# Performance work log

Measured on AMD Instinct MI355X. Metric: run time of the kernel, lower is better.

## Reference

```python
import jax, jax.numpy as jnp
import numpy as np

BATCH = 64
FEAT = 2048          # backbone.out_features (ResNet-50)
C = 112              # bottleneck_dim = number of concepts
E = 512              # concept_emb_dim
NUM_CLASSES = 345


def setup_inputs() -> dict:
    key = jax.random.key(0)
    ks = jax.random.split(key, 7)
    s_emb = 1.0 / np.sqrt(FEAT)
    s_p = 1.0 / np.sqrt(2 * E)
    s_h = 1.0 / np.sqrt(C * E)
    return {
        "x": jax.random.normal(ks[0], (BATCH, FEAT), jnp.float32),
        "W_emb": jax.random.normal(ks[1], (C, FEAT, 2 * E), jnp.float32) * s_emb,
        "b_emb": jax.random.normal(ks[2], (C, 2 * E), jnp.float32) * s_emb,
        "W_pint": jax.random.normal(ks[3], (C, 2 * E), jnp.float32) * s_p,
        "b_pint": jax.random.normal(ks[4], (C,), jnp.float32) * s_p,
        "W_head": jax.random.normal(ks[5], (C * E, NUM_CLASSES), jnp.float32) * s_h,
        "b_head": jax.random.normal(ks[6], (NUM_CLASSES,), jnp.float32) * s_h,
    }


def reference(x, W_emb, b_emb, W_pint, b_pint, W_head, b_head):
    # Batched version of the per-concept Linear loop: [B,C,2E]
    embeddings = jnp.einsum("bf,cfe->bce", x, W_emb) + b_emb
    positive_embs = embeddings[..., :E]   # [B,C,E]
    negative_embs = embeddings[..., E:]   # [B,C,E]
    # Per-concept Linear(2E, 1) -> [B,C]
    p_int_logits = jnp.einsum("bce,ce->bc", embeddings, W_pint) + b_pint
    p_int_pos = jax.nn.sigmoid(p_int_logits)              # [B,C]
    p = p_int_pos[..., None]
    mixed_embs = p * positive_embs + (1.0 - p) * negative_embs  # [B,C,E]
    flattened = mixed_embs.reshape(mixed_embs.shape[0], -1)     # [B, C*E]
    final_preds = flattened @ W_head + b_head                   # [B, num_classes]
    return (final_preds, flattened, p_int_pos)
```

## Files before the change

kernel.cpp:

```cpp
#include <hip/hip_runtime.h>

typedef __attribute__((ext_vector_type(4))) float  f4;
typedef __attribute__((ext_vector_type(8))) short  bf16x8;
typedef __attribute__((ext_vector_type(4))) float  f32x4;
typedef __attribute__((ext_vector_type(4))) unsigned short us4;
typedef __attribute__((ext_vector_type(2))) unsigned int u32x2;
typedef __attribute__((ext_vector_type(4))) unsigned int u32x4;

#define BATCH 64
#define FEAT 2048
#define NC_C 112
#define TE 1024
#define EE 512
#define NCLS 345
#define NCLSP 352
#define KHEAD 57344

__device__ __forceinline__ unsigned short f2bf(float f) {
    unsigned u = __float_as_uint(f);
    unsigned r = (u + 0x7FFFu + ((u >> 16) & 1u)) >> 16;
    return (unsigned short)r;
}
__device__ __forceinline__ float bf2f(unsigned short h) {
    return __uint_as_float(((unsigned)h) << 16);
}
__device__ __forceinline__ unsigned cvtpk(float a, float b) {
    unsigned r;
    asm("v_cvt_pk_bf16_f32 %0, %1, %2" : "=v"(r) : "v"(a), "v"(b));
    return r;
}

__global__ __launch_bounds__(256) void k_emb(
    const float* __restrict__ x, const float* __restrict__ W_emb,
    unsigned short* __restrict__ pbe)
{
    __shared__ __align__(16) unsigned short Alds[64 * 40];
    __shared__ __align__(16) unsigned short Blds[128 * 40];

    const int tid = threadIdx.x;
    const int bid = blockIdx.x;
    const int c  = bid >> 6;
    const int nt = (bid >> 3) & 7;
    const int ks = bid & 7;
    const int n0 = nt * 128;
    const int kofs = ks * 256;
    const float* __restrict__ Wc = W_emb + (size_t)c * (FEAT * TE);

    const int w = tid >> 6, l = tid & 63;
    const int mbase = (w & 1) * 32, nbase = (w >> 1) * 64;

    const int a_row = tid >> 3;
    const int a_k4  = (tid & 7) * 4;
    const int b_kp  = tid >> 4;
    const int b_n4  = (tid & 15) * 4;

    const float* __restrict__ axp = x + (size_t)a_row * FEAT + kofs + a_k4;
    const float* __restrict__ bpp = Wc + (size_t)(kofs + 2 * b_kp) * TE + n0 + b_n4;

    unsigned short* __restrict__ aw0 = &Alds[a_row * 40 + a_k4];
    unsigned short* __restrict__ aw1 = &Alds[(a_row + 32) * 40 + a_k4];
    const int koct = b_kp >> 2, klo = (2 * b_kp) & 7;

    auto ke_load = [&](f4& A0, f4& A1, f4& B0, f4& B1, f4& B2, f4& B3, int kstep) {
        const float* ax_ = axp + kstep * 32;
        A0 = *(const f4*)ax_;
        A1 = *(const f4*)(ax_ + 32 * FEAT);
        const float* bp_ = bpp + (size_t)kstep * 32 * TE;
        B0 = *(const f4*)bp_;         B1 = *(const f4*)(bp_ + TE);
        B2 = *(const f4*)(bp_ + 64);  B3 = *(const f4*)(bp_ + TE + 64);
    };
    auto ke_write = [&](const f4& A0, const f4& A1, const f4& B0, const f4& B1,
                        const f4& B2, const f4& B3) {
        u32x2 v0, v1;
        v0[0] = cvtpk(A0[0], A0[1]); v0[1] = cvtpk(A0[2], A0[3]);
        v1[0] = cvtpk(A1[0], A1[1]); v1[1] = cvtpk(A1[2], A1[3]);
        *(u32x2*)aw0 = v0;
        *(u32x2*)aw1 = v1;
#pragma unroll
        for (int i = 0; i < 4; ++i) {
            int n = b_n4 + i;
            *(unsigned*)&Blds[n * 40 + (((koct ^ ((n >> 2) & 3)) << 3) | klo)] =
                cvtpk(B0[i], B1[i]);
            n += 64;
            *(unsigned*)&Blds[n * 40 + (((koct ^ ((n >> 2) & 3)) << 3) | klo)] =
                cvtpk(B2[i], B3[i]);
        }
    };

    f32x4 acc[2][4];
#pragma unroll
    for (int i = 0; i < 2; ++i)
#pragma unroll
        for (int j = 0; j < 4; ++j) acc[i][j] = (f32x4){0.f, 0.f, 0.f, 0.f};

    auto ke_mfma = [&]() {
        bf16x8 af[2], bfr[4];
#pragma unroll
        for (int si = 0; si < 2; ++si)
            af[si] = *(const bf16x8*)&Alds[(mbase + si * 16 + (l & 15)) * 40 + (l >> 4) * 8];
#pragma unroll
        for (int nf = 0; nf < 4; ++nf) {
            int n = nbase + nf * 16 + (l & 15);
            bfr[nf] = *(const bf16x8*)&Blds[n * 40 + (((l >> 4) ^ ((n >> 2) & 3)) << 3)];
        }
#pragma unroll
        for (int si = 0; si < 2; ++si)
#pragma unroll
            for (int nf = 0; nf < 4; ++nf)
                acc[si][nf] = __builtin_amdgcn_mfma_f32_16x16x32_bf16(
                    af[si], bfr[nf], acc[si][nf], 0, 0, 0);
    };

    f4 a0, a1, p0, p1, p2, p3;
    ke_load(a0, a1, p0, p1, p2, p3, 0);

    for (int s = 0; s < 8; ++s) {
        __syncthreads();
        ke_write(a0, a1, p0, p1, p2, p3);
        __syncthreads();
        if (s < 7) ke_load(a0, a1, p0, p1, p2, p3, s + 1);
        ke_mfma();
    }

#pragma unroll
    for (int si = 0; si < 2; ++si)
#pragma unroll
        for (int nf = 0; nf < 4; ++nf) {
            const int nl = nbase + nf * 16 + (l & 15);
            const int ng = n0 + nl;
#pragma unroll
            for (int r = 0; r < 4; ++r) {
                const int m = mbase + si * 16 + (l >> 4) * 4 + r;
                pbe[((size_t)(ks * 64 + m) * NC_C + c) * TE + ng] = f2bf(acc[si][nf][r]);
            }
        }
}

__global__ __launch_bounds__(256) void k_mix(
    const unsigned short* __restrict__ pbe, const float* __restrict__ b_emb,
    const float* __restrict__ W_pint, const float* __restrict__ b_pint,
    float* __restrict__ flat_out, float* __restrict__ p_out)
{
    const int tid = threadIdx.x;
    const int l = tid & 63, w = tid >> 6;
    const int pidx = blockIdx.x * 4 + w;
    const int b = pidx / NC_C, c = pidx - b * NC_C;

    float vals[16];
#pragma unroll
    for (int i = 0; i < 4; ++i) {
        const f4 bi = *(const f4*)&b_emb[c * TE + 4 * l + 256 * i];
#pragma unroll
        for (int j = 0; j < 4; ++j) vals[4 * i + j] = bi[j];
    }
#pragma unroll
    for (int ksl = 0; ksl < 8; ++ksl) {
        const unsigned short* __restrict__ rp =
            pbe + ((size_t)(ksl * 64 + b) * NC_C + c) * TE;
#pragma unroll
        for (int i = 0; i < 4; ++i) {
            us4 u = *(const us4*)&rp[4 * l + 256 * i];
#pragma unroll
            for (int j = 0; j < 4; ++j) vals[4 * i + j] += bf2f(u[j]);
        }
    }

    const float* __restrict__ wp = W_pint + c * TE;
    float dot = 0.f;
#pragma unroll
    for (int i = 0; i < 4; ++i) {
        const f4 wv = *(const f4*)&wp[4 * l + 256 * i];
#pragma unroll
        for (int j = 0; j < 4; ++j) dot += vals[4 * i + j] * wv[j];
    }
#pragma unroll
    for (int m = 32; m >= 1; m >>= 1) dot += __shfl_xor(dot, m);
    const float logit = dot + b_pint[c];
    const float p = 1.f / (1.f + __expf(-logit));
    if (l == 0) p_out[b * NC_C + c] = p;

    float* __restrict__ fo = flat_out + (size_t)b * KHEAD + c * EE;
#pragma unroll
    for (int i = 0; i < 2; ++i) {
        f4 m;
#pragma unroll
        for (int j = 0; j < 4; ++j)
            m[j] = p * vals[i * 4 + j] + (1.f - p) * vals[(i + 2) * 4 + j];
        *(f4*)&fo[4 * l + 256 * i] = m;
    }
}

__global__ __launch_bounds__(256) void k_head(
    const float* __restrict__ flat, const float* __restrict__ W_head,
    float* __restrict__ pbuf, int nsteps)
{
    __shared__ __align__(16) unsigned short Blds[NCLSP * 40];

    const int tid = threadIdx.x;
    const int w = tid >> 6, l = tid & 63;
    const int k0 = blockIdx.x * (nsteps * 32);

    f32x4 acc[22];
#pragma unroll
    for (int i = 0; i < 22; ++i) acc[i] = (f32x4){0.f, 0.f, 0.f, 0.f};

    for (int s = 0; s < nsteps; ++s) {
        const int kb = k0 + s * 32;
        __syncthreads();
        for (int idx = tid; idx < 32 * NCLSP; idx += 256) {
            const int k = idx / NCLSP;
            const int n = idx - k * NCLSP;
            const float v = (n < NCLS) ? W_head[(size_t)(kb + k) * NCLS + n] : 0.f;
            Blds[n * 40 + ((((k >> 3) ^ ((n >> 2) & 3)) << 3) | (k & 7))] = f2bf(v);
        }
        __syncthreads();

        const float* __restrict__ ap =
            flat + (size_t)(w * 16 + (l & 15)) * KHEAD + kb + (l >> 4) * 8;
        f4 af0 = *(const f4*)ap;
        f4 af1 = *(const f4*)(ap + 4);
        u32x4 pq;
        pq[0] = cvtpk(af0[0], af0[1]); pq[1] = cvtpk(af0[2], af0[3]);
        pq[2] = cvtpk(af1[0], af1[1]); pq[3] = cvtpk(af1[2], af1[3]);
        bf16x8 a = __builtin_bit_cast(bf16x8, pq);

#pragma unroll
        for (int nf = 0; nf < 22; ++nf) {
            const int n = nf * 16 + (l & 15);
            bf16x8 bfr = *(const bf16x8*)&Blds[n * 40 + (((l >> 4) ^ ((n >> 2) & 3)) << 3)];
            acc[nf] = __builtin_amdgcn_mfma_f32_16x16x32_bf16(a, bfr, acc[nf], 0, 0, 0);
        }
    }

    float* __restrict__ pb = pbuf + (size_t)blockIdx.x * (64 * NCLSP);
#pragma unroll
    for (int nf = 0; nf < 22; ++nf) {
        const int n = nf * 16 + (l & 15);
#pragma unroll
        for (int r = 0; r < 4; ++r) {
            const int row = w * 16 + (l >> 4) * 4 + r;
            pb[row * NCLSP + n] = acc[nf][r];
        }
    }
}

__global__ __launch_bounds__(256) void k_reduce(
    const float* __restrict__ pbuf, const float* __restrict__ b_head,
    float* __restrict__ final_out, int nb)
{
    const int i = blockIdx.x * 256 + threadIdx.x;
    if (i >= BATCH * NCLS) return;
    const int m = i / NCLS, n = i - m * NCLS;
    float s = b_head[n];
    for (int p = 0; p < nb; ++p)
        s += pbuf[((size_t)p * 64 + m) * NCLSP + n];
    final_out[i] = s;
}

extern "C" void kernel_launch(void* const* d_in, const int* in_sizes, int n_in,
                              void* d_out, int out_size, void* d_ws, size_t ws_size,
                              hipStream_t stream) {
    const float* x      = (const float*)d_in[0];
    const float* W_emb  = (const float*)d_in[1];
    const float* b_emb  = (const float*)d_in[2];
    const float* W_pint = (const float*)d_in[3];
    const float* b_pint = (const float*)d_in[4];
    const float* W_head = (const float*)d_in[5];
    const float* b_head = (const float*)d_in[6];

    float* out       = (float*)d_out;
    float* final_out = out;
    float* flat      = out + BATCH * NCLS;
    float* p_out     = out + BATCH * NCLS + BATCH * KHEAD;

    unsigned short* pbe = (unsigned short*)d_ws;
    float* pbuf_h = (float*)((char*)d_ws + (size_t)120 * 1024 * 1024);

    const int NB = 224, nsteps = 8;

    k_emb<<<NC_C * 8 * 8, 256, 0, stream>>>(x, W_emb, pbe);
    k_mix<<<(BATCH * NC_C) / 4, 256, 0, stream>>>(pbe, b_emb, W_pint, b_pint, flat, p_out);
    k_head<<<NB, 256, 0, stream>>>(flat, W_head, pbuf_h, nsteps);
    k_reduce<<<(BATCH * NCLS + 255) / 256, 256, 0, stream>>>(pbuf_h, b_head, final_out, NB);
}
```

Measured before the change: 478.7 us.

## Widen k_emb tiles to full 1024-column N per block, load A directly

Restructures the embedding GEMM so each 512-thread block covers all 1024 output columns of one concept and K-slice, rather than a 128-column tile. The A operand (x) is no longer staged in LDS; each wave loads and converts it to bf16 straight from global memory into registers. The aim is to cut redundant x reads and block count while raising MFMA work per LDS load. In exchange the grid shrinks to 896 blocks, LDS grows to about 80KB per block, and register pressure rises (128 accumulator floats plus 16 staged f4), which may reduce occupancy.

New measurement: 503.1 us. 5.1% more time.

```diff
diff --git a/kernel.cpp b/kernel.cpp
--- a/kernel.cpp
+++ b/kernel.cpp
@@ -30,108 +30,98 @@
     return r;
 }
 
-__global__ __launch_bounds__(256) void k_emb(
+__global__ __launch_bounds__(512) void k_emb(
     const float* __restrict__ x, const float* __restrict__ W_emb,
     unsigned short* __restrict__ pbe)
 {
-    __shared__ __align__(16) unsigned short Alds[64 * 40];
-    __shared__ __align__(16) unsigned short Blds[128 * 40];
+    __shared__ __align__(16) unsigned short Blds[1024 * 40];
 
     const int tid = threadIdx.x;
-    const int bid = blockIdx.x;
-    const int c  = bid >> 6;
-    const int nt = (bid >> 3) & 7;
-    const int ks = bid & 7;
-    const int n0 = nt * 128;
-    const int kofs = ks * 256;
-    const float* __restrict__ Wc = W_emb + (size_t)c * (FEAT * TE);
+    const int c  = blockIdx.x >> 3;
+    const int ks = blockIdx.x & 7;
+    const float* __restrict__ Wc =
+        W_emb + (size_t)c * (FEAT * TE) + (size_t)(ks * 256) * TE;
 
     const int w = tid >> 6, l = tid & 63;
-    const int mbase = (w & 1) * 32, nbase = (w >> 1) * 64;
-
-    const int a_row = tid >> 3;
-    const int a_k4  = (tid & 7) * 4;
-    const int b_kp  = tid >> 4;
-    const int b_n4  = (tid & 15) * 4;
-
-    const float* __restrict__ axp = x + (size_t)a_row * FEAT + kofs + a_k4;
-    const float* __restrict__ bpp = Wc + (size_t)(kofs + 2 * b_kp) * TE + n0 + b_n4;
-
-    unsigned short* __restrict__ aw0 = &Alds[a_row * 40 + a_k4];
-    unsigned short* __restrict__ aw1 = &Alds[(a_row + 32) * 40 + a_k4];
-    const int koct = b_kp >> 2, klo = (2 * b_kp) & 7;
-
-    auto ke_load = [&](f4& A0, f4& A1, f4& B0, f4& B1, f4& B2, f4& B3, int kstep) {
-        const float* ax_ = axp + kstep * 32;
-        A0 = *(const f4*)ax_;
-        A1 = *(const f4*)(ax_ + 32 * FEAT);
-        const float* bp_ = bpp + (size_t)kstep * 32 * TE;
-        B0 = *(const f4*)bp_;         B1 = *(const f4*)(bp_ + TE);
-        B2 = *(const f4*)(bp_ + 64);  B3 = *(const f4*)(bp_ + TE + 64);
+    const int lm = l & 15, kg = l >> 4;
+    const int wn = w * 128;
+
+    const int no = l;
+    const int koct_w = w >> 1;
+    const int klo_w  = (w & 1) * 4;
+
+    f32x4 acc[4][8];
+#pragma unroll
+    for (int mf = 0; mf < 4; ++mf)
+#pragma unroll
+        for (int nf = 0; nf < 8; ++nf) acc[mf][nf] = (f32x4){0.f, 0.f, 0.f, 0.f};
+
+    auto loadB = [&](f4* R, int s) {
+        const float* base = Wc + (size_t)(s * 32 + 4 * w) * TE + no * 4;
+#pragma unroll
+        for (int kk = 0; kk < 4; ++kk)
+#pragma unroll
+            for (int g = 0; g < 4; ++g)
+                R[g * 4 + kk] = *(const f4*)(base + (size_t)kk * TE + g * 256);
     };
-    auto ke_write = [&](const f4& A0, const f4& A1, const f4& B0, const f4& B1,
-                        const f4& B2, const f4& B3) {
-        u32x2 v0, v1;
-        v0[0] = cvtpk(A0[0], A0[1]); v0[1] = cvtpk(A0[2], A0[3]);
-        v1[0] = cvtpk(A1[0], A1[1]); v1[1] = cvtpk(A1[2], A1[3]);
-        *(u32x2*)aw0 = v0;
-        *(u32x2*)aw1 = v1;
-#pragma unroll
-        for (int i = 0; i < 4; ++i) {
-            int n = b_n4 + i;
-            *(unsigned*)&Blds[n * 40 + (((koct ^ ((n >> 2) & 3)) << 3) | klo)] =
-                cvtpk(B0[i], B1[i]);
-            n += 64;
-            *(unsigned*)&Blds[n * 40 + (((koct ^ ((n >> 2) & 3)) << 3) | klo)] =
-                cvtpk(B2[i], B3[i]);
-        }
+    auto writeB = [&](const f4* R) {
+#pragma unroll
+        for (int g = 0; g < 4; ++g)
+#pragma unroll
+            for (int ni = 0; ni < 4; ++ni) {
+                const int n = g * 256 + no * 4 + ni;
+                u32x2 v;
+                v[0] = cvtpk(R[g * 4 + 0][ni], R[g * 4 + 1][ni]);
+                v[1] = cvtpk(R[g * 4 + 2][ni], R[g * 4 + 3][ni]);
+                *(u32x2*)&Blds[n * 40 + (((koct_w ^ ((n >> 2) & 3)) << 3) | klo_w)] = v;
+            }
     };
 
-    f32x4 acc[2][4];
-#pragma unroll
-    for (int i = 0; i < 2; ++i)
-#pragma unroll
-        for (int j = 0; j < 4; ++j) acc[i][j] = (f32x4){0.f, 0.f, 0.f, 0.f};
-
-    auto ke_mfma = [&]() {
-        bf16x8 af[2], bfr[4];
-#pragma unroll
-        for (int si = 0; si < 2; ++si)
-            af[si] = *(const bf16x8*)&Alds[(mbase + si * 16 + (l & 15)) * 40 + (l >> 4) * 8];
-#pragma unroll
-        for (int nf = 0; nf < 4; ++nf) {
-            int n = nbase + nf * 16 + (l & 15);
-            bfr[nf] = *(const bf16x8*)&Blds[n * 40 + (((l >> 4) ^ ((n >> 2) & 3)) << 3)];
-        }
-#pragma unroll
-        for (int si = 0; si < 2; ++si)
-#pragma unroll
-            for (int nf = 0; nf < 4; ++nf)
-                acc[si][nf] = __builtin_amdgcn_mfma_f32_16x16x32_bf16(
-                    af[si], bfr[nf], acc[si][nf], 0, 0, 0);
+    auto compute = [&](int s) {
+        const int kofs = ks * 256 + s * 32;
+        bf16x8 afr[4];
+#pragma unroll
+        for (int mf = 0; mf < 4; ++mf) {
+            const float* ap = x + (size_t)(mf * 16 + lm) * FEAT + kofs + kg * 8;
+            const f4 a0 = *(const f4*)ap;
+            const f4 a1 = *(const f4*)(ap + 4);
+            u32x4 q;
+            q[0] = cvtpk(a0[0], a0[1]); q[1] = cvtpk(a0[2], a0[3]);
+            q[2] = cvtpk(a1[0], a1[1]); q[3] = cvtpk(a1[2], a1[3]);
+            afr[mf] = __builtin_bit_cast(bf16x8, q);
+        }
+#pragma unroll
+        for (int nf = 0; nf < 8; ++nf) {
+            const int n = wn + nf * 16 + lm;
+            const bf16x8 bfr =
+                *(const bf16x8*)&Blds[n * 40 + (((kg ^ ((n >> 2) & 3)) << 3))];
+#pragma unroll
+            for (int mf = 0; mf < 4; ++mf)
+                acc[mf][nf] = __builtin_amdgcn_mfma_f32_16x16x32_bf16(
+                    afr[mf], bfr, acc[mf][nf], 0, 0, 0);
+        }
     };
 
-    f4 a0, a1, p0, p1, p2, p3;
-    ke_load(a0, a1, p0, p1, p2, p3, 0);
+    f4 R[16];
+    loadB(R, 0);
 
     for (int s = 0; s < 8; ++s) {
         __syncthreads();
-        ke_write(a0, a1, p0, p1, p2, p3);
-        __syncthreads();
-        if (s < 7) ke_load(a0, a1, p0, p1, p2, p3, s + 1);
-        ke_mfma();
-    }
-
-#pragma unroll
-    for (int si = 0; si < 2; ++si)
-#pragma unroll
-        for (int nf = 0; nf < 4; ++nf) {
-            const int nl = nbase + nf * 16 + (l & 15);
-            const int ng = n0 + nl;
+        writeB(R);
+        __syncthreads();
+        if (s < 7) loadB(R, s + 1);
+        compute(s);
+    }
+
+#pragma unroll
+    for (int mf = 0; mf < 4; ++mf)
+#pragma unroll
+        for (int nf = 0; nf < 8; ++nf) {
+            const int e = wn + nf * 16 + lm;
 #pragma unroll
             for (int r = 0; r < 4; ++r) {
-                const int m = mbase + si * 16 + (l >> 4) * 4 + r;
-                pbe[((size_t)(ks * 64 + m) * NC_C + c) * TE + ng] = f2bf(acc[si][nf][r]);
+                const int m = mf * 16 + kg * 4 + r;
+                pbe[((size_t)(ks * 64 + m) * NC_C + c) * TE + e] = f2bf(acc[mf][nf][r]);
             }
         }
 }
@@ -278,7 +268,7 @@
 
     const int NB = 224, nsteps = 8;
 
-    k_emb<<<NC_C * 8 * 8, 256, 0, stream>>>(x, W_emb, pbe);
+    k_emb<<<NC_C * 8, 512, 0, stream>>>(x, W_emb, pbe);
     k_mix<<<(BATCH * NC_C) / 4, 256, 0, stream>>>(pbe, b_emb, W_pint, b_pint, flat, p_out);
     k_head<<<NB, 256, 0, stream>>>(flat, W_head, pbuf_h, nsteps);
     k_reduce<<<(BATCH * NCLS + 255) / 256, 256, 0, stream>>>(pbuf_h, b_head, final_out, NB);
```
